# Kernel optimization log

Hardware: AMD Instinct MI355X
Metric: run time of the kernel (lower is better)

The kernel has to match this reference:

```python
import jax, jax.numpy as jnp
import numpy as np

N = 100000          # num nodes
E = 3200000         # num edges (avg degree 32)
CLIN = 64           # clinical feature dim
MEL_SHAPE = (32, 40)  # flattened -> 1280
MEL = 1280
H = 128             # hidden_dim
C = 4               # num_classes


def setup_inputs() -> dict:
    key = jax.random.key(0)
    ks = jax.random.split(key, 14)
    s = lambda d: 1.0 / np.sqrt(d)
    inp = {
        "clinical": jax.random.normal(ks[0], (N, CLIN), jnp.float32),
        "mel": jax.random.normal(ks[1], (N,) + MEL_SHAPE, jnp.float32),
        "edge_index": jax.random.randint(ks[2], (2, E), 0, N, dtype=jnp.int32),
        # mel_linear
        "Wm": jax.random.normal(ks[3], (H, MEL), jnp.float32) * s(MEL),
        "bm": jnp.zeros((H,), jnp.float32),
        # concat_linear (in = H + CLIN)
        "Wc": jax.random.normal(ks[4], (H, H + CLIN), jnp.float32) * s(H + CLIN),
        "bc": jnp.zeros((H,), jnp.float32),
        # sage1: lin_l (neighbors, with bias), lin_r (root, no bias)
        "Wl1": jax.random.normal(ks[5], (H, H), jnp.float32) * s(H),
        "bl1": jnp.zeros((H,), jnp.float32),
        "Wr1": jax.random.normal(ks[6], (H, H), jnp.float32) * s(H),
        # sage2
        "Wl2": jax.random.normal(ks[7], (C, H), jnp.float32) * s(H),
        "bl2": jnp.zeros((C,), jnp.float32),
        "Wr2": jax.random.normal(ks[8], (C, H), jnp.float32) * s(H),
    }
    return inp


def _sage_conv(x, src, dst, Wl, bl, Wr):
    """PyG SAGEConv with mean aggregation:
    out = lin_l(mean_{j in N(i)} x_j) + lin_r(x_i).
    src = edge_index[0] (message source), dst = edge_index[1] (target).
    """
    msg_sum = jax.ops.segment_sum(x[src], dst, num_segments=N)  # [N, d]
    cnt = jax.ops.segment_sum(jnp.ones((src.shape[0], 1), x.dtype), dst,
                              num_segments=N)                    # [N, 1]
    agg = msg_sum / jnp.maximum(cnt, 1.0)
    return agg @ Wl.T + bl + x @ Wr.T


def reference(clinical, mel, edge_index, Wm, bm, Wc, bc,
              Wl1, bl1, Wr1, Wl2, bl2, Wr2):
    src, dst = edge_index[0], edge_index[1]
    mel_flat = mel.reshape(mel.shape[0], -1)                 # [N, 1280]
    mel_h = jax.nn.relu(mel_flat @ Wm.T + bm)                # [N, H]
    x = jnp.concatenate([clinical, mel_h], axis=1)           # [N, CLIN+H]
    x = jax.nn.relu(x @ Wc.T + bc)                           # [N, H]
    x = jax.nn.relu(_sage_conv(x, src, dst, Wl1, bl1, Wr1))  # [N, H]
    x = _sage_conv(x, src, dst, Wl2, bl2, Wr2)               # [N, C]
    return x
```

## Files before the change

### kernel.cpp

```cpp
#include <hip/hip_runtime.h>
#include <hip/hip_bf16.h>
#include <stdint.h>

#define NN   100000
#define EE   3200000
#define HD   128

typedef short v8s __attribute__((ext_vector_type(8)));
typedef float v4f __attribute__((ext_vector_type(4)));

__device__ __forceinline__ unsigned short f2bf(float f){
  union { float f; unsigned int i; } v; v.f = f;
  unsigned int r = v.i + 0x7fffu + ((v.i >> 16) & 1u);
  return (unsigned short)(r >> 16);
}
__device__ __forceinline__ uint4 pack8(float4 lo, float4 hi){
  uint4 r;
  r.x = (unsigned)f2bf(lo.x) | ((unsigned)f2bf(lo.y) << 16);
  r.y = (unsigned)f2bf(lo.z) | ((unsigned)f2bf(lo.w) << 16);
  r.z = (unsigned)f2bf(hi.x) | ((unsigned)f2bf(hi.y) << 16);
  r.w = (unsigned)f2bf(hi.z) | ((unsigned)f2bf(hi.w) << 16);
  return r;
}
__device__ __forceinline__ void acc8(float* a, uint4 u){
  union {unsigned int i; float f;} t;
  t.i = u.x << 16;         a[0] += t.f;
  t.i = u.x & 0xffff0000u; a[1] += t.f;
  t.i = u.y << 16;         a[2] += t.f;
  t.i = u.y & 0xffff0000u; a[3] += t.f;
  t.i = u.z << 16;         a[4] += t.f;
  t.i = u.z & 0xffff0000u; a[5] += t.f;
  t.i = u.w << 16;         a[6] += t.f;
  t.i = u.w & 0xffff0000u; a[7] += t.f;
}

__global__ void k_zero(int* p, int n){
  int i = blockIdx.x*blockDim.x + threadIdx.x; if (i < n) p[i] = 0;
}
__global__ void k_histrank(const int* __restrict__ dst, int* __restrict__ cnt,
                           int* __restrict__ rank, int e){
  int i = blockIdx.x*blockDim.x + threadIdx.x;
  if (i < e) rank[i] = atomicAdd(&cnt[dst[i]], 1);
}
__global__ __launch_bounds__(1024)
void k_scan1(const int* __restrict__ cnt, int* __restrict__ offs, int* __restrict__ blksum, int n){
  __shared__ int lds[1024];
  int t = threadIdx.x; int i = blockIdx.x*1024 + t;
  int v = (i < n) ? cnt[i] : 0;
  lds[t] = v; __syncthreads();
  for (int s = 1; s < 1024; s <<= 1){
    int add = (t >= s) ? lds[t-s] : 0;
    __syncthreads();
    lds[t] += add;
    __syncthreads();
  }
  if (i < n) offs[i] = lds[t] - v;
  if (t == 1023) blksum[blockIdx.x] = lds[1023];
}
__global__ __launch_bounds__(128)
void k_scan2(int* __restrict__ blksum, int nb){
  __shared__ int lds[128];
  int t = threadIdx.x;
  int v = (t < nb) ? blksum[t] : 0;
  lds[t] = v; __syncthreads();
  for (int s = 1; s < 128; s <<= 1){
    int a = (t >= s) ? lds[t-s] : 0;
    __syncthreads();
    lds[t] += a;
    __syncthreads();
  }
  if (t < nb) blksum[t] = lds[t] - v;
}
__global__ __launch_bounds__(1024)
void k_scan3(int* __restrict__ offs, const int* __restrict__ blksum, int n){
  int i = blockIdx.x*1024 + threadIdx.x;
  if (i < n) offs[i] += blksum[blockIdx.x];
}
__global__ void k_place(const int* __restrict__ src, const int* __restrict__ dst,
                        const int* __restrict__ offs, const int* __restrict__ rank,
                        int* __restrict__ ssrc, int e){
  int i = blockIdx.x*blockDim.x + threadIdx.x;
  if (i < e) ssrc[offs[dst[i]] + rank[i]] = src[i];
}

__device__ __forceinline__ void gemm_issue(int t, int T0, int M, int gm, int r0, int c8,
    const void* __restrict__ A0, int lda0, int a0f32,
    const void* __restrict__ A1, int lda1, int a1f32,
    const float* __restrict__ B0, int ldb0,
    const float* __restrict__ B1, int ldb1,
    uint4* as, uint4* bs)
{
  const void* Ag; const float* Bg; int la, lb, ko, af32;
  if (t < T0){ Ag = A0; la = lda0; af32 = a0f32; Bg = B0; lb = ldb0; ko = t*64; }
  else       { Ag = A1; la = lda1; af32 = a1f32; Bg = B1; lb = ldb1; ko = (t-T0)*64; }
#pragma unroll
  for (int p = 0; p < 4; p++){
    int row  = r0 + p*32;
    int grow = gm + row;
    if (grow < M){
      if (af32){
        const float* ap = (const float*)Ag + (size_t)grow*la + ko + c8;
        as[p] = pack8(*(const float4*)ap, *(const float4*)(ap + 4));
      } else {
        as[p] = *(const uint4*)((const unsigned short*)Ag + (size_t)grow*la + ko + c8);
      }
    } else {
      as[p] = make_uint4(0u,0u,0u,0u);
    }
    const float* bp = Bg + (size_t)row*lb + ko + c8;
    bs[p] = pack8(*(const float4*)bp, *(const float4*)(bp + 4));
  }
}

__global__ __launch_bounds__(256)
void k_gemm(int M,
            const void* __restrict__ A0, int lda0, int K0, int a0f32,
            const void* __restrict__ A1, int lda1, int K1, int a1f32,
            const float* __restrict__ B0, int ldb0,
            const float* __restrict__ B1, int ldb1,
            const float* __restrict__ bias, int do_relu,
            unsigned short* __restrict__ C, int ldc)
{
  __shared__ unsigned short Abuf[128*72];
  __shared__ unsigned short Bbuf[128*72];
  const int tid = threadIdx.x;
  const int gm  = blockIdx.x * 128;
  const int T0  = K0 >> 6;
  const int T   = (K0 + K1) >> 6;

  const int r0 = tid >> 3;
  const int c8 = (tid & 7) * 8;

  const int lane = tid & 63;
  const int w  = tid >> 6;
  const int wm = w >> 1, wn = w & 1;
  const int l15 = lane & 15, q = lane >> 4;

  v4f acc[4][4];
#pragma unroll
  for (int mi = 0; mi < 4; mi++)
#pragma unroll
    for (int ni = 0; ni < 4; ni++){ v4f z = {0.f,0.f,0.f,0.f}; acc[mi][ni] = z; }

  uint4 aS[4], bS[4];
  gemm_issue(0, T0, M, gm, r0, c8, A0, lda0, a0f32, A1, lda1, a1f32,
             B0, ldb0, B1, ldb1, aS, bS);

  for (int t = 0; t < T; ++t){
#pragma unroll
    for (int p = 0; p < 4; p++){
      int row = r0 + p*32;
      *(uint4*)(Abuf + row*72 + c8) = aS[p];
      *(uint4*)(Bbuf + row*72 + c8) = bS[p];
    }
    __syncthreads();
    if (t + 1 < T)
      gemm_issue(t+1, T0, M, gm, r0, c8, A0, lda0, a0f32, A1, lda1, a1f32,
                 B0, ldb0, B1, ldb1, aS, bS);
#pragma unroll
    for (int kk = 0; kk < 64; kk += 32){
      v8s af[4], bf[4];
#pragma unroll
      for (int mi = 0; mi < 4; mi++)
        af[mi] = *(const v8s*)(Abuf + (wm*64 + mi*16 + l15)*72 + kk + q*8);
#pragma unroll
      for (int ni = 0; ni < 4; ni++)
        bf[ni] = *(const v8s*)(Bbuf + (wn*64 + ni*16 + l15)*72 + kk + q*8);
#pragma unroll
      for (int mi = 0; mi < 4; mi++)
#pragma unroll
        for (int ni = 0; ni < 4; ni++)
          acc[mi][ni] = __builtin_amdgcn_mfma_f32_16x16x32_bf16(af[mi], bf[ni], acc[mi][ni], 0, 0, 0);
    }
    __syncthreads();
  }

#pragma unroll
  for (int ni = 0; ni < 4; ni++){
    int n = wn*64 + ni*16 + l15;
    float bv = bias ? bias[n] : 0.0f;
#pragma unroll
    for (int mi = 0; mi < 4; mi++){
#pragma unroll
      for (int r = 0; r < 4; r++){
        int row = gm + wm*64 + mi*16 + q*4 + r;
        if (row < M){
          float v = acc[mi][ni][r] + bv;
          if (do_relu) v = v > 0.f ? v : 0.f;
          C[(size_t)row*ldc + n] = f2bf(v);
        }
      }
    }
  }
}

__global__ __launch_bounds__(256)
void k_agg1(const int* __restrict__ offs, const int* __restrict__ cnt,
            const int* __restrict__ ssrc,
            const unsigned short* __restrict__ y1,
            const unsigned short* __restrict__ z1,
            const float* __restrict__ Wl2,
            const float* __restrict__ Wr2,
            const float* __restrict__ bl2,
            float* __restrict__ y2, float* __restrict__ r2, int n)
{
  int wid  = (blockIdx.x * blockDim.x + threadIdx.x) >> 6;
  int lane = threadIdx.x & 63;
  if (wid >= n) return;
  int start = offs[wid];
  int deg   = cnt[wid];
  const uint4* y1q = (const uint4*)y1;
  const int g = lane >> 4;
  const int c = lane & 15;

  float a[8];
#pragma unroll
  for (int j = 0; j < 8; j++) a[j] = 0.f;

  for (int base = 0; base < deg; base += 64){
    int idx = base + lane;
    int sl  = (idx < deg) ? ssrc[start + idx] : 0;
    int m   = deg - base; if (m > 64) m = 64;
    int quads = (m + 3) >> 2;
    int tq = 0;
    for (; tq + 2 <= quads; tq += 2){
      int e0 = tq*4 + g, e1 = e0 + 4;
      int i0 = e0 < m ? e0 : m-1;
      int i1 = e1 < m ? e1 : m-1;
      int s0 = __shfl(sl, i0, 64);
      int s1 = __shfl(sl, i1, 64);
      uint4 u0 = y1q[(size_t)s0*16 + c];
      uint4 u1 = y1q[(size_t)s1*16 + c];
      if (e0 < m) acc8(a, u0);
      if (e1 < m) acc8(a, u1);
    }
    if (tq < quads){
      int e0 = tq*4 + g;
      int i0 = e0 < m ? e0 : m-1;
      int s0 = __shfl(sl, i0, 64);
      uint4 u0 = y1q[(size_t)s0*16 + c];
      if (e0 < m) acc8(a, u0);
    }
  }
#pragma unroll
  for (int j = 0; j < 8; j++){
    a[j] += __shfl_xor(a[j], 16, 64);
    a[j] += __shfl_xor(a[j], 32, 64);
  }

  float scale = 1.0f / (float)(deg > 0 ? deg : 1);
  uint4 zu = ((const uint4*)z1)[(size_t)wid*16 + c];
  float x8[8];
  {
    union {unsigned int i; float f;} t;
    t.i = zu.x << 16;         x8[0] = t.f;
    t.i = zu.x & 0xffff0000u; x8[1] = t.f;
    t.i = zu.y << 16;         x8[2] = t.f;
    t.i = zu.y & 0xffff0000u; x8[3] = t.f;
    t.i = zu.z << 16;         x8[4] = t.f;
    t.i = zu.z & 0xffff0000u; x8[5] = t.f;
    t.i = zu.w << 16;         x8[6] = t.f;
    t.i = zu.w & 0xffff0000u; x8[7] = t.f;
  }
#pragma unroll
  for (int j = 0; j < 8; j++){
    float v = a[j]*scale + x8[j];
    x8[j] = v > 0.f ? v : 0.f;
  }

  float pl[4], pr[4];
#pragma unroll
  for (int cc = 0; cc < 4; cc++){
    const float* wl = Wl2 + cc*128 + 8*c;
    const float* wr = Wr2 + cc*128 + 8*c;
    float4 wl0 = *(const float4*)wl, wl1 = *(const float4*)(wl + 4);
    float4 wr0 = *(const float4*)wr, wr1 = *(const float4*)(wr + 4);
    pl[cc] = x8[0]*wl0.x + x8[1]*wl0.y + x8[2]*wl0.z + x8[3]*wl0.w
           + x8[4]*wl1.x + x8[5]*wl1.y + x8[6]*wl1.z + x8[7]*wl1.w;
    pr[cc] = x8[0]*wr0.x + x8[1]*wr0.y + x8[2]*wr0.z + x8[3]*wr0.w
           + x8[4]*wr1.x + x8[5]*wr1.y + x8[6]*wr1.z + x8[7]*wr1.w;
  }
#pragma unroll
  for (int off = 8; off >= 1; off >>= 1){
#pragma unroll
    for (int cc = 0; cc < 4; cc++){
      pl[cc] += __shfl_xor(pl[cc], off, 64);
      pr[cc] += __shfl_xor(pr[cc], off, 64);
    }
  }
  if (lane == 0){
    float4 o; o.x = pl[0]; o.y = pl[1]; o.z = pl[2]; o.w = pl[3];
    *(float4*)(y2 + (size_t)wid*4) = o;
    float4 b = *(const float4*)bl2;
    float4 p; p.x = pr[0]+b.x; p.y = pr[1]+b.y; p.z = pr[2]+b.z; p.w = pr[3]+b.w;
    *(float4*)(r2 + (size_t)wid*4) = p;
  }
}

__global__ __launch_bounds__(256)
void k_agg2(const int* __restrict__ offs, const int* __restrict__ cnt,
            const int* __restrict__ ssrc,
            const float* __restrict__ y2, const float* __restrict__ r2,
            float* __restrict__ out, int n)
{
  int wid  = (blockIdx.x * blockDim.x + threadIdx.x) >> 6;
  int lane = threadIdx.x & 63;
  if (wid >= n) return;
  int start = offs[wid], deg = cnt[wid];
  float a0 = 0.f, a1 = 0.f, a2 = 0.f, a3 = 0.f;
  for (int base = 0; base < deg; base += 64){
    int idx = base + lane;
    if (idx < deg){
      int s = ssrc[start + idx];
      float4 v = *(const float4*)(y2 + (size_t)s*4);
      a0 += v.x; a1 += v.y; a2 += v.z; a3 += v.w;
    }
  }
#pragma unroll
  for (int off = 32; off >= 1; off >>= 1){
    a0 += __shfl_xor(a0, off, 64);
    a1 += __shfl_xor(a1, off, 64);
    a2 += __shfl_xor(a2, off, 64);
    a3 += __shfl_xor(a3, off, 64);
  }
  if (lane == 0){
    float sc = 1.0f / (float)(deg > 0 ? deg : 1);
    float4 r = *(const float4*)(r2 + (size_t)wid*4);
    float4 o;
    o.x = a0*sc + r.x; o.y = a1*sc + r.y; o.z = a2*sc + r.z; o.w = a3*sc + r.w;
    *(float4*)(out + (size_t)wid*4) = o;
  }
}

extern "C" void kernel_launch(void* const* d_in, const int* in_sizes, int n_in,
                              void* d_out, int out_size, void* d_ws, size_t ws_size,
                              hipStream_t stream)
{
  (void)in_sizes; (void)n_in; (void)out_size; (void)ws_size;
  const float* clinical = (const float*)d_in[0];
  const float* mel      = (const float*)d_in[1];
  const int*   ei       = (const int*)d_in[2];
  const float* Wm  = (const float*)d_in[3];
  const float* bm  = (const float*)d_in[4];
  const float* Wc  = (const float*)d_in[5];
  const float* bc  = (const float*)d_in[6];
  const float* Wl1 = (const float*)d_in[7];
  const float* bl1 = (const float*)d_in[8];
  const float* Wr1 = (const float*)d_in[9];
  const float* Wl2 = (const float*)d_in[10];
  const float* bl2 = (const float*)d_in[11];
  const float* Wr2 = (const float*)d_in[12];
  const int* src = ei;
  const int* dst = ei + EE;

  char* w = (char*)d_ws;
  auto alloc = [&](size_t sz){ void* p = (void*)w; w += (sz + 255) & ~(size_t)255; return p; };
  unsigned short* mel_h = (unsigned short*)alloc((size_t)NN*HD*2);
  unsigned short* x     = (unsigned short*)alloc((size_t)NN*HD*2);
  unsigned short* z1    = (unsigned short*)alloc((size_t)NN*HD*2);
  int*   ssrc   = (int*)alloc((size_t)EE*4);
  int*   rank   = (int*)alloc((size_t)EE*4);
  int*   cnt    = (int*)alloc((size_t)NN*4);
  int*   offs   = (int*)alloc((size_t)NN*4);
  int*   blksum = (int*)alloc(4096);
  float* y2     = (float*)alloc((size_t)NN*4*4);
  float* r2     = (float*)alloc((size_t)NN*4*4);

  k_zero<<<(NN+255)/256, 256, 0, stream>>>(cnt, NN);
  k_histrank<<<(EE+255)/256, 256, 0, stream>>>(dst, cnt, rank, EE);
  int nblk = (NN + 1023) / 1024;
  k_scan1<<<nblk, 1024, 0, stream>>>(cnt, offs, blksum, NN);
  k_scan2<<<1, 128, 0, stream>>>(blksum, nblk);
  k_scan3<<<nblk, 1024, 0, stream>>>(offs, blksum, NN);
  k_place<<<(EE+255)/256, 256, 0, stream>>>(src, dst, offs, rank, ssrc, EE);

  int gmb = (NN + 127) / 128;
  k_gemm<<<gmb, 256, 0, stream>>>(NN, mel, 1280, 1280, 1, nullptr, 0, 0, 0,
                                  Wm, 1280, nullptr, 0, bm, 1, mel_h, HD);
  k_gemm<<<gmb, 256, 0, stream>>>(NN, clinical, 64, 64, 1, mel_h, HD, HD, 0,
                                  Wc, 192, Wc + 64, 192, bc, 1, x, HD);
  unsigned short* y1 = mel_h;
  k_gemm<<<gmb, 256, 0, stream>>>(NN, x, HD, HD, 0, nullptr, 0, 0, 0,
                                  Wl1, HD, nullptr, 0, nullptr, 0, y1, HD);
  k_gemm<<<gmb, 256, 0, stream>>>(NN, x, HD, HD, 0, nullptr, 0, 0, 0,
                                  Wr1, HD, nullptr, 0, bl1, 0, z1, HD);

  k_agg1<<<(NN+3)/4, 256, 0, stream>>>(offs, cnt, ssrc, y1, z1, Wl2, Wr2, bl2, y2, r2, NN);
  k_agg2<<<(NN+3)/4, 256, 0, stream>>>(offs, cnt, ssrc, y2, r2, (float*)d_out, NN);
}
```

Measured before the change: 1.241 ms.

## Pre-convert weights to bf16 and split edge histogram into 8 sub-counters

A new kernel converts the GEMM weight matrices to bf16 once, so each GEMM block loads bf16 B tiles directly instead of loading fp32 and packing per tile. The histogram and rank step now spreads atomics across 8 per-lane-slot count arrays, which cuts contention on popular destination nodes. It also uses int4 vectorized loads, then adds a per-node sub-offset pass that is used during placement. This trades extra launches and an 8x larger count buffer to zero and read for fewer contended atomics and less repeated weight conversion.

```diff
diff --git a/kernel.cpp b/kernel.cpp
--- a/kernel.cpp
+++ b/kernel.cpp
@@ -14,12 +14,15 @@
   unsigned int r = v.i + 0x7fffu + ((v.i >> 16) & 1u);
   return (unsigned short)(r >> 16);
 }
+__device__ __forceinline__ unsigned cvt2(float a, float b){
+  return (unsigned)f2bf(a) | ((unsigned)f2bf(b) << 16);
+}
 __device__ __forceinline__ uint4 pack8(float4 lo, float4 hi){
   uint4 r;
-  r.x = (unsigned)f2bf(lo.x) | ((unsigned)f2bf(lo.y) << 16);
-  r.y = (unsigned)f2bf(lo.z) | ((unsigned)f2bf(lo.w) << 16);
-  r.z = (unsigned)f2bf(hi.x) | ((unsigned)f2bf(hi.y) << 16);
-  r.w = (unsigned)f2bf(hi.z) | ((unsigned)f2bf(hi.w) << 16);
+  r.x = cvt2(lo.x, lo.y);
+  r.y = cvt2(lo.z, lo.w);
+  r.z = cvt2(hi.x, hi.y);
+  r.w = cvt2(hi.z, hi.w);
   return r;
 }
 __device__ __forceinline__ void acc8(float* a, uint4 u){
@@ -34,13 +37,52 @@
   t.i = u.w & 0xffff0000u; a[7] += t.f;
 }
 
+__global__ __launch_bounds__(256)
+void k_cvtw(const float* __restrict__ Wm, const float* __restrict__ Wc,
+            const float* __restrict__ Wl1, const float* __restrict__ Wr1,
+            unsigned short* __restrict__ Wmb, unsigned short* __restrict__ Wcb,
+            unsigned short* __restrict__ Wl1b, unsigned short* __restrict__ Wr1b)
+{
+  int p = blockIdx.x*blockDim.x + threadIdx.x;
+  const float* s; unsigned* d; int off;
+  if      (p <  81920){ s = Wm;  d = (unsigned*)Wmb;  off = p; }
+  else if (p <  94208){ s = Wc;  d = (unsigned*)Wcb;  off = p -  81920; }
+  else if (p < 102400){ s = Wl1; d = (unsigned*)Wl1b; off = p -  94208; }
+  else if (p < 110592){ s = Wr1; d = (unsigned*)Wr1b; off = p - 102400; }
+  else return;
+  float2 v = ((const float2*)s)[off];
+  d[off] = cvt2(v.x, v.y);
+}
+
 __global__ void k_zero(int* p, int n){
   int i = blockIdx.x*blockDim.x + threadIdx.x; if (i < n) p[i] = 0;
 }
-__global__ void k_histrank(const int* __restrict__ dst, int* __restrict__ cnt,
-                           int* __restrict__ rank, int e){
+__global__ __launch_bounds__(256)
+void k_histrank(const int* __restrict__ dst, int* __restrict__ cnt2,
+                int* __restrict__ rank, int e4){
   int i = blockIdx.x*blockDim.x + threadIdx.x;
-  if (i < e) rank[i] = atomicAdd(&cnt[dst[i]], 1);
+  if (i >= e4) return;
+  int4 d4 = ((const int4*)dst)[i];
+  int b = (4*i) & 7;
+  int4 r4;
+  r4.x = atomicAdd(&cnt2[(b+0)*NN + d4.x], 1);
+  r4.y = atomicAdd(&cnt2[(b+1)*NN + d4.y], 1);
+  r4.z = atomicAdd(&cnt2[(b+2)*NN + d4.z], 1);
+  r4.w = atomicAdd(&cnt2[(b+3)*NN + d4.w], 1);
+  ((int4*)rank)[i] = r4;
+}
+__global__ __launch_bounds__(256)
+void k_suboff(int* __restrict__ cnt2, int* __restrict__ cnt, int n){
+  int d = blockIdx.x*blockDim.x + threadIdx.x;
+  if (d >= n) return;
+  int s = 0;
+#pragma unroll
+  for (int k = 0; k < 8; k++){
+    int v = cnt2[k*n + d];
+    cnt2[k*n + d] = s;
+    s += v;
+  }
+  cnt[d] = s;
 }
 __global__ __launch_bounds__(1024)
 void k_scan1(const int* __restrict__ cnt, int* __restrict__ offs, int* __restrict__ blksum, int n){
@@ -76,21 +118,30 @@
   int i = blockIdx.x*1024 + threadIdx.x;
   if (i < n) offs[i] += blksum[blockIdx.x];
 }
-__global__ void k_place(const int* __restrict__ src, const int* __restrict__ dst,
-                        const int* __restrict__ offs, const int* __restrict__ rank,
-                        int* __restrict__ ssrc, int e){
+__global__ __launch_bounds__(256)
+void k_place(const int* __restrict__ src, const int* __restrict__ dst,
+             const int* __restrict__ offs, const int* __restrict__ rank,
+             const int* __restrict__ suboff, int* __restrict__ ssrc, int e4){
   int i = blockIdx.x*blockDim.x + threadIdx.x;
-  if (i < e) ssrc[offs[dst[i]] + rank[i]] = src[i];
+  if (i >= e4) return;
+  int4 s4 = ((const int4*)src)[i];
+  int4 d4 = ((const int4*)dst)[i];
+  int4 r4 = ((const int4*)rank)[i];
+  int b = (4*i) & 7;
+  ssrc[offs[d4.x] + suboff[(b+0)*NN + d4.x] + r4.x] = s4.x;
+  ssrc[offs[d4.y] + suboff[(b+1)*NN + d4.y] + r4.y] = s4.y;
+  ssrc[offs[d4.z] + suboff[(b+2)*NN + d4.z] + r4.z] = s4.z;
+  ssrc[offs[d4.w] + suboff[(b+3)*NN + d4.w] + r4.w] = s4.w;
 }
 
 __device__ __forceinline__ void gemm_issue(int t, int T0, int M, int gm, int r0, int c8,
     const void* __restrict__ A0, int lda0, int a0f32,
     const void* __restrict__ A1, int lda1, int a1f32,
-    const float* __restrict__ B0, int ldb0,
-    const float* __restrict__ B1, int ldb1,
+    const unsigned short* __restrict__ B0, int ldb0,
+    const unsigned short* __restrict__ B1, int ldb1,
     uint4* as, uint4* bs)
 {
-  const void* Ag; const float* Bg; int la, lb, ko, af32;
+  const void* Ag; const unsigned short* Bg; int la, lb, ko, af32;
   if (t < T0){ Ag = A0; la = lda0; af32 = a0f32; Bg = B0; lb = ldb0; ko = t*64; }
   else       { Ag = A1; la = lda1; af32 = a1f32; Bg = B1; lb = ldb1; ko = (t-T0)*64; }
 #pragma unroll
@@ -107,8 +158,7 @@
     } else {
       as[p] = make_uint4(0u,0u,0u,0u);
     }
-    const float* bp = Bg + (size_t)row*lb + ko + c8;
-    bs[p] = pack8(*(const float4*)bp, *(const float4*)(bp + 4));
+    bs[p] = *(const uint4*)(Bg + (size_t)row*lb + ko + c8);
   }
 }
 
@@ -116,8 +166,8 @@
 void k_gemm(int M,
             const void* __restrict__ A0, int lda0, int K0, int a0f32,
             const void* __restrict__ A1, int lda1, int K1, int a1f32,
-            const float* __restrict__ B0, int ldb0,
-            const float* __restrict__ B1, int ldb1,
+            const unsigned short* __restrict__ B0, int ldb0,
+            const unsigned short* __restrict__ B1, int ldb1,
             const float* __restrict__ bias, int do_relu,
             unsigned short* __restrict__ C, int ldc)
 {
@@ -360,30 +410,38 @@
   unsigned short* z1    = (unsigned short*)alloc((size_t)NN*HD*2);
   int*   ssrc   = (int*)alloc((size_t)EE*4);
   int*   rank   = (int*)alloc((size_t)EE*4);
+  int*   cnt2   = (int*)alloc((size_t)NN*8*4);
   int*   cnt    = (int*)alloc((size_t)NN*4);
   int*   offs   = (int*)alloc((size_t)NN*4);
   int*   blksum = (int*)alloc(4096);
   float* y2     = (float*)alloc((size_t)NN*4*4);
   float* r2     = (float*)alloc((size_t)NN*4*4);
-
-  k_zero<<<(NN+255)/256, 256, 0, stream>>>(cnt, NN);
-  k_histrank<<<(EE+255)/256, 256, 0, stream>>>(dst, cnt, rank, EE);
+  unsigned short* Wmb  = (unsigned short*)alloc((size_t)128*1280*2);
+  unsigned short* Wcb  = (unsigned short*)alloc((size_t)128*192*2);
+  unsigned short* Wl1b = (unsigned short*)alloc((size_t)128*128*2);
+  unsigned short* Wr1b = (unsigned short*)alloc((size_t)128*128*2);
+
+  k_cvtw<<<432, 256, 0, stream>>>(Wm, Wc, Wl1, Wr1, Wmb, Wcb, Wl1b, Wr1b);
+
+  k_zero<<<(NN*8+255)/256, 256, 0, stream>>>(cnt2, NN*8);
+  k_histrank<<<(EE/4+255)/256, 256, 0, stream>>>(dst, cnt2, rank, EE/4);
+  k_suboff<<<(NN+255)/256, 256, 0, stream>>>(cnt2, cnt, NN);
   int nblk = (NN + 1023) / 1024;
   k_scan1<<<nblk, 1024, 0, stream>>>(cnt, offs, blksum, NN);
   k_scan2<<<1, 128, 0, stream>>>(blksum, nblk);
   k_scan3<<<nblk, 1024, 0, stream>>>(offs, blksum, NN);
-  k_place<<<(EE+255)/256, 256, 0, stream>>>(src, dst, offs, rank, ssrc, EE);
+  k_place<<<(EE/4+255)/256, 256, 0, stream>>>(src, dst, offs, rank, cnt2, ssrc, EE/4);
 
   int gmb = (NN + 127) / 128;
   k_gemm<<<gmb, 256, 0, stream>>>(NN, mel, 1280, 1280, 1, nullptr, 0, 0, 0,
-                                  Wm, 1280, nullptr, 0, bm, 1, mel_h, HD);
+                                  Wmb, 1280, nullptr, 0, bm, 1, mel_h, HD);
   k_gemm<<<gmb, 256, 0, stream>>>(NN, clinical, 64, 64, 1, mel_h, HD, HD, 0,
-                                  Wc, 192, Wc + 64, 192, bc, 1, x, HD);
+                                  Wcb, 192, Wcb + 64, 192, bc, 1, x, HD);
   unsigned short* y1 = mel_h;
   k_gemm<<<gmb, 256, 0, stream>>>(NN, x, HD, HD, 0, nullptr, 0, 0, 0,
-                                  Wl1, HD, nullptr, 0, nullptr, 0, y1, HD);
+                                  Wl1b, HD, nullptr, 0, nullptr, 0, y1, HD);
   k_gemm<<<gmb, 256, 0, stream>>>(NN, x, HD, HD, 0, nullptr, 0, 0, 0,
-                                  Wr1, HD, nullptr, 0, bl1, 0, z1, HD);
+                                  Wr1b, HD, nullptr, 0, bl1, 0, z1, HD);
 
   k_agg1<<<(NN+3)/4, 256, 0, stream>>>(offs, cnt, ssrc, y1, z1, Wl2, Wr2, bl2, y2, r2, NN);
   k_agg2<<<(NN+3)/4, 256, 0, stream>>>(offs, cnt, ssrc, y2, r2, (float*)d_out, NN);
```

Measured after the change: 1.382 ms. +11.3%, slower.
